# Optimization experiments

Measured on AMD Instinct MI355X. Metric: run time of the kernel, lower is better.

Reference implementation:

```python
import jax, jax.numpy as jnp
import numpy as np

B, N, D, E = 4, 16384, 128, 1048576  # batch, nodes/graph, hidden, total edges


def setup_inputs() -> dict:
    key = jax.random.key(0)
    k0, k1, k2, k3, k4, k5, k6 = jax.random.split(key, 7)
    x = jax.random.normal(k0, (B, N, D), dtype=jnp.float32)
    W = jax.random.normal(k1, (D, D), dtype=jnp.float32) * 0.05  # 'random_normal' init
    b = jax.random.normal(k2, (D,), dtype=jnp.float32) * 0.05
    edge_b = jax.random.randint(k3, (E,), 0, B, dtype=jnp.int32)
    edge_row = jax.random.randint(k4, (E,), 0, N, dtype=jnp.int32)
    edge_col = jax.random.randint(k5, (E,), 0, N, dtype=jnp.int32)
    edge_vals = jax.random.uniform(k6, (E,), dtype=jnp.float32)
    return {"x": x, "W": W, "b": b, "edge_b": edge_b, "edge_row": edge_row,
            "edge_col": edge_col, "edge_vals": edge_vals, "k": 2}


def reference(x, W, b, edge_b, edge_row, edge_col, edge_vals, k):
    # adj is a batched sparse [B, N, N]; edges stored as (batch, row, col, val) COO.
    seg_row = edge_b * N + edge_row  # flattened destination id in [0, B*N)
    # in_degrees = sum_j |adj[b, i, j]|
    deg = jax.ops.segment_sum(jnp.abs(edge_vals), seg_row, num_segments=B * N)
    deg = deg.reshape(B, N)
    norm = jnp.power(deg + 1e-6, -0.5)[..., None]          # [B, N, 1]
    norm_k = jnp.power(norm, k)                             # computed but unused (faithful to source)
    support = jnp.einsum('bnd,de->bne', x, W)               # x @ W
    y = (support * norm).reshape(B * N, D)                  # pre-normalized features
    # SpMM: out[b, i] = sum_{(b,i,j)} adj_val * y[b, j]
    msgs = y[edge_b * N + edge_col] * edge_vals[:, None]    # [E, D] gather + scale
    agg = jax.ops.segment_sum(msgs, seg_row, num_segments=B * N).reshape(B, N, D)
    return jax.nn.relu(agg * norm + b)
```

## Files before the change

### kernel.cpp

```cpp
#include <hip/hip_runtime.h>
#include <stdint.h>

#define B_ 4
#define N_ 16384
#define D_ 128
#define E_ 1048576
#define BN_ 65536
#define NBKT 256
#define NBLK 256
#define SCANB 64

typedef __attribute__((ext_vector_type(8))) short short8;
typedef __attribute__((ext_vector_type(4))) float floatx4;

static constexpr size_t OFF_Y      = 0;
static constexpr size_t OFF_PACK2  = 16777216;
static constexpr size_t OFF_HIST   = OFF_PACK2 + 8388608;
static constexpr size_t OFF_CURSOR = OFF_HIST + 262144;
static constexpr size_t OFF_NORM   = OFF_CURSOR + 262144;
static constexpr size_t OFF_BSUM   = OFF_NORM + 262144;
static constexpr size_t OFF_WH     = OFF_BSUM + 1024;
static constexpr size_t OFF_WL     = OFF_WH + 32768;

__device__ __forceinline__ uint32_t rne16(uint32_t u) {
    return (u + 0x7FFFu + ((u >> 16) & 1u)) >> 16;
}
__device__ __forceinline__ void bf16split(float f, uint16_t& h, uint16_t& l) {
    uint32_t hb = rne16(__float_as_uint(f));
    h = (uint16_t)hb;
    float r = f - __uint_as_float(hb << 16);
    l = (uint16_t)rne16(__float_as_uint(r));
}

__global__ __launch_bounds__(1024) void k_hist(const int* __restrict__ eb,
                                               const int* __restrict__ er,
                                               const float* __restrict__ Wg,
                                               uint32_t* __restrict__ histM,
                                               uint16_t* __restrict__ WhG,
                                               uint16_t* __restrict__ WlG) {
    __shared__ uint32_t h[NBKT];
    int t = threadIdx.x;
    if (t < NBKT) h[t] = 0;
    __syncthreads();
    if (blockIdx.x < 16) {
        int g = blockIdx.x * 1024 + t;
        float w = Wg[g];
        uint16_t hh, ll;
        bf16split(w, hh, ll);
        int k = g >> 7, n = g & 127;
        int o = ((k >> 3) * 128 + n) * 8 + (k & 7);
        WhG[o] = hh;
        WlG[o] = ll;
    }
    int vbase = blockIdx.x * 1024 + t;
    int4 b4 = ((const int4*)eb)[vbase];
    int4 r4 = ((const int4*)er)[vbase];
    atomicAdd(&h[(uint32_t)(b4.x * N_ + r4.x) >> 8], 1u);
    atomicAdd(&h[(uint32_t)(b4.y * N_ + r4.y) >> 8], 1u);
    atomicAdd(&h[(uint32_t)(b4.z * N_ + r4.z) >> 8], 1u);
    atomicAdd(&h[(uint32_t)(b4.w * N_ + r4.w) >> 8], 1u);
    __syncthreads();
    if (t < NBKT) histM[t * NBLK + blockIdx.x] = h[t];
}

__global__ __launch_bounds__(1024) void k_scan1(uint32_t* __restrict__ histM,
                                                uint32_t* __restrict__ bsum) {
    __shared__ uint32_t s[1024];
    int t = threadIdx.x;
    int g = blockIdx.x * 1024 + t;
    uint32_t v = histM[g];
    s[t] = v;
    __syncthreads();
    for (int off = 1; off < 1024; off <<= 1) {
        uint32_t a = (t >= off) ? s[t - off] : 0u;
        __syncthreads();
        s[t] += a;
        __syncthreads();
    }
    histM[g] = s[t] - v;
    if (t == 1023) bsum[blockIdx.x] = s[1023];
}

__global__ void k_scan2(uint32_t* bsum) {
    if (threadIdx.x == 0) {
        uint32_t acc = 0;
        for (int i = 0; i < SCANB; ++i) { uint32_t v = bsum[i]; bsum[i] = acc; acc += v; }
    }
}

__global__ __launch_bounds__(1024) void k_scan3(uint32_t* __restrict__ histM,
                                                const uint32_t* __restrict__ bsum) {
    int g = blockIdx.x * 1024 + threadIdx.x;
    histM[g] += bsum[blockIdx.x];
}

__global__ __launch_bounds__(1024) void k_scatter(const int* __restrict__ eb,
                                                  const int* __restrict__ er,
                                                  const int* __restrict__ ec,
                                                  const float* __restrict__ ev,
                                                  const uint32_t* __restrict__ histM,
                                                  uint2* __restrict__ pack1) {
    __shared__ uint32_t cur[NBKT];
    int t = threadIdx.x;
    if (t < NBKT) cur[t] = histM[t * NBLK + blockIdx.x];
    __syncthreads();
    int vbase = blockIdx.x * 1024 + t;
    int4   b4 = ((const int4*)eb)[vbase];
    int4   r4 = ((const int4*)er)[vbase];
    int4   c4 = ((const int4*)ec)[vbase];
    float4 v4 = ((const float4*)ev)[vbase];
    {
        uint32_t key = (uint32_t)(b4.x * N_ + r4.x);
        uint32_t pos = atomicAdd(&cur[key >> 8], 1u);
        pack1[pos] = make_uint2(((key & 255u) << 14) | (uint32_t)c4.x, __float_as_uint(v4.x));
    }
    {
        uint32_t key = (uint32_t)(b4.y * N_ + r4.y);
        uint32_t pos = atomicAdd(&cur[key >> 8], 1u);
        pack1[pos] = make_uint2(((key & 255u) << 14) | (uint32_t)c4.y, __float_as_uint(v4.y));
    }
    {
        uint32_t key = (uint32_t)(b4.z * N_ + r4.z);
        uint32_t pos = atomicAdd(&cur[key >> 8], 1u);
        pack1[pos] = make_uint2(((key & 255u) << 14) | (uint32_t)c4.z, __float_as_uint(v4.z));
    }
    {
        uint32_t key = (uint32_t)(b4.w * N_ + r4.w);
        uint32_t pos = atomicAdd(&cur[key >> 8], 1u);
        pack1[pos] = make_uint2(((key & 255u) << 14) | (uint32_t)c4.w, __float_as_uint(v4.w));
    }
}

__global__ __launch_bounds__(1024) void k_build(const uint32_t* __restrict__ histM,
                                                const uint2* __restrict__ pack1,
                                                uint2* __restrict__ pack2,
                                                uint32_t* __restrict__ cursor,
                                                float* __restrict__ norm) {
    __shared__ uint32_t cnt[NBKT];
    __shared__ float    dsum[NBKT];
    __shared__ uint32_t scn[NBKT];
    __shared__ uint32_t rcur[NBKT];
    int t = threadIdx.x;
    int bkt = blockIdx.x;
    uint32_t bstart = histM[bkt * NBLK];
    uint32_t bend = (bkt == NBKT - 1) ? E_ : histM[(bkt + 1) * NBLK];
    if (t < NBKT) { cnt[t] = 0; dsum[t] = 0.f; }
    __syncthreads();
    for (uint32_t i = bstart + t; i < bend; i += 1024) {
        uint2 p = pack1[i];
        uint32_t nl = p.x >> 14;
        atomicAdd(&cnt[nl], 1u);
        atomicAdd(&dsum[nl], fabsf(__uint_as_float(p.y)));
    }
    __syncthreads();
    if (t < NBKT) scn[t] = cnt[t];
    __syncthreads();
    for (int off = 1; off < NBKT; off <<= 1) {
        uint32_t a = 0;
        if (t < NBKT && t >= off) a = scn[t - off];
        __syncthreads();
        if (t < NBKT) scn[t] += a;
        __syncthreads();
    }
    if (t < NBKT) {
        uint32_t incl = scn[t];
        uint32_t excl = incl - cnt[t];
        rcur[t] = bstart + excl;
        cursor[bkt * NBKT + t] = bstart + incl;
        norm[bkt * NBKT + t] = rsqrtf(dsum[t] + 1e-6f);
    }
    __syncthreads();
    uint32_t colbase = (uint32_t)(bkt >> 6) * N_;
    for (uint32_t i = bstart + t; i < bend; i += 1024) {
        uint2 p = pack1[i];
        uint32_t nl = p.x >> 14;
        uint32_t pos = atomicAdd(&rcur[nl], 1u);
        pack2[pos] = make_uint2(colbase + (p.x & 0x3FFFu), p.y);
    }
}

__global__ __launch_bounds__(256) void k_matmul_mfma(const float* __restrict__ x,
                                                     const uint16_t* __restrict__ WhG,
                                                     const uint16_t* __restrict__ WlG,
                                                     const float* __restrict__ norm,
                                                     uint32_t* __restrict__ ybf) {
    __shared__ short WhS[16384];
    __shared__ short WlS[16384];
    __shared__ short XhS[4096];
    __shared__ short XlS[4096];
    __shared__ float normS[32];
    int tid = threadIdx.x;
    int row0 = blockIdx.x * 32;

    {
        const uint4* whg = (const uint4*)WhG;
        const uint4* wlg = (const uint4*)WlG;
        uint4* whs = (uint4*)WhS;
        uint4* wls = (uint4*)WlS;
#pragma unroll
        for (int i = 0; i < 8; ++i) {
            whs[i * 256 + tid] = whg[i * 256 + tid];
            wls[i * 256 + tid] = wlg[i * 256 + tid];
        }
    }
#pragma unroll
    for (int cc = 0; cc < 2; ++cc) {
        int c = cc * 256 + tid;
        int m = c & 31, kk = c >> 5;
        const float4* xp = (const float4*)(x + (size_t)(row0 + m) * D_ + kk * 8);
        float4 f0 = xp[0], f1 = xp[1];
        union { short8 v; uint16_t s[8]; } uh, ul;
        bf16split(f0.x, uh.s[0], ul.s[0]); bf16split(f0.y, uh.s[1], ul.s[1]);
        bf16split(f0.z, uh.s[2], ul.s[2]); bf16split(f0.w, uh.s[3], ul.s[3]);
        bf16split(f1.x, uh.s[4], ul.s[4]); bf16split(f1.y, uh.s[5], ul.s[5]);
        bf16split(f1.z, uh.s[6], ul.s[6]); bf16split(f1.w, uh.s[7], ul.s[7]);
        ((short8*)XhS)[c] = uh.v;
        ((short8*)XlS)[c] = ul.v;
    }
    if (tid < 32) normS[tid] = norm[row0 + tid];
    __syncthreads();

    int lane = tid & 63;
    int wv = tid >> 6;
    int quad = lane >> 4;
    int l15 = lane & 15;
    int wcol0 = wv * 32;
    floatx4 acc[2][2] = {};
    const short8* Xh8 = (const short8*)XhS;
    const short8* Xl8 = (const short8*)XlS;
    const short8* Wh8 = (const short8*)WhS;
    const short8* Wl8 = (const short8*)WlS;
#pragma unroll
    for (int ks = 0; ks < 4; ++ks) {
        int kkq = ks * 4 + quad;
        short8 ah0 = Xh8[kkq * 32 + l15];
        short8 ah1 = Xh8[kkq * 32 + 16 + l15];
        short8 al0 = Xl8[kkq * 32 + l15];
        short8 al1 = Xl8[kkq * 32 + 16 + l15];
        short8 bh0 = Wh8[kkq * 128 + wcol0 + l15];
        short8 bh1 = Wh8[kkq * 128 + wcol0 + 16 + l15];
        short8 bl0 = Wl8[kkq * 128 + wcol0 + l15];
        short8 bl1 = Wl8[kkq * 128 + wcol0 + 16 + l15];
        acc[0][0] = __builtin_amdgcn_mfma_f32_16x16x32_bf16(ah0, bh0, acc[0][0], 0, 0, 0);
        acc[0][1] = __builtin_amdgcn_mfma_f32_16x16x32_bf16(ah0, bh1, acc[0][1], 0, 0, 0);
        acc[1][0] = __builtin_amdgcn_mfma_f32_16x16x32_bf16(ah1, bh0, acc[1][0], 0, 0, 0);
        acc[1][1] = __builtin_amdgcn_mfma_f32_16x16x32_bf16(ah1, bh1, acc[1][1], 0, 0, 0);
        acc[0][0] = __builtin_amdgcn_mfma_f32_16x16x32_bf16(ah0, bl0, acc[0][0], 0, 0, 0);
        acc[0][1] = __builtin_amdgcn_mfma_f32_16x16x32_bf16(ah0, bl1, acc[0][1], 0, 0, 0);
        acc[1][0] = __builtin_amdgcn_mfma_f32_16x16x32_bf16(ah1, bl0, acc[1][0], 0, 0, 0);
        acc[1][1] = __builtin_amdgcn_mfma_f32_16x16x32_bf16(ah1, bl1, acc[1][1], 0, 0, 0);
        acc[0][0] = __builtin_amdgcn_mfma_f32_16x16x32_bf16(al0, bh0, acc[0][0], 0, 0, 0);
        acc[0][1] = __builtin_amdgcn_mfma_f32_16x16x32_bf16(al0, bh1, acc[0][1], 0, 0, 0);
        acc[1][0] = __builtin_amdgcn_mfma_f32_16x16x32_bf16(al1, bh0, acc[1][0], 0, 0, 0);
        acc[1][1] = __builtin_amdgcn_mfma_f32_16x16x32_bf16(al1, bh1, acc[1][1], 0, 0, 0);
    }

#pragma unroll
    for (int rt = 0; rt < 2; ++rt) {
#pragma unroll
        for (int ct = 0; ct < 2; ++ct) {
            floatx4 v = acc[rt][ct];
            int rbase = rt * 16 + quad * 4;
            int cp = (wcol0 + ct * 16) / 2 + (l15 >> 1);
#pragma unroll
            for (int r = 0; r < 4; ++r) {
                float mine = v[r] * normS[rbase + r];
                float oth = __shfl_xor(mine, 1, 64);
                uint32_t a = __float_as_uint((lane & 1) ? oth : mine);
                uint32_t b = __float_as_uint((lane & 1) ? mine : oth);
                uint32_t packed = rne16(a) | (rne16(b) << 16);
                bool doit = ((lane & 1) == 0) ? (r < 2) : (r >= 2);
                if (doit)
                    ybf[(size_t)(row0 + rbase + r) * 64 + cp] = packed;
            }
        }
    }
}

__global__ __launch_bounds__(256) void k_spmm(const uint32_t* __restrict__ cursor,
                                              const uint2* __restrict__ pack,
                                              const uint32_t* __restrict__ ybf,
                                              const float* __restrict__ norm,
                                              const float* __restrict__ bias,
                                              float* __restrict__ out) {
    int node = blockIdx.x * 4 + (threadIdx.x >> 6);
    int lane = threadIdx.x & 63;
    uint32_t end = cursor[node];
    uint32_t start = (node == 0) ? 0u : cursor[node - 1];
    float2 a0 = {0.f,0.f}, a1 = {0.f,0.f}, a2 = {0.f,0.f}, a3 = {0.f,0.f};
    uint32_t e = start;
    for (; e + 8 <= end; e += 8) {
        uint2 p0 = pack[e + 0]; uint2 p1 = pack[e + 1];
        uint2 p2 = pack[e + 2]; uint2 p3 = pack[e + 3];
        uint2 p4 = pack[e + 4]; uint2 p5 = pack[e + 5];
        uint2 p6 = pack[e + 6]; uint2 p7 = pack[e + 7];
        uint32_t u0 = ybf[(size_t)p0.x * 64 + lane];
        uint32_t u1 = ybf[(size_t)p1.x * 64 + lane];
        uint32_t u2 = ybf[(size_t)p2.x * 64 + lane];
        uint32_t u3 = ybf[(size_t)p3.x * 64 + lane];
        uint32_t u4 = ybf[(size_t)p4.x * 64 + lane];
        uint32_t u5 = ybf[(size_t)p5.x * 64 + lane];
        uint32_t u6 = ybf[(size_t)p6.x * 64 + lane];
        uint32_t u7 = ybf[(size_t)p7.x * 64 + lane];
        float v0 = __uint_as_float(p0.y), v1 = __uint_as_float(p1.y);
        float v2 = __uint_as_float(p2.y), v3 = __uint_as_float(p3.y);
        float v4 = __uint_as_float(p4.y), v5 = __uint_as_float(p5.y);
        float v6 = __uint_as_float(p6.y), v7 = __uint_as_float(p7.y);
        a0.x = fmaf(v0, __uint_as_float(u0 << 16), a0.x);
        a0.y = fmaf(v0, __uint_as_float(u0 & 0xFFFF0000u), a0.y);
        a1.x = fmaf(v1, __uint_as_float(u1 << 16), a1.x);
        a1.y = fmaf(v1, __uint_as_float(u1 & 0xFFFF0000u), a1.y);
        a2.x = fmaf(v2, __uint_as_float(u2 << 16), a2.x);
        a2.y = fmaf(v2, __uint_as_float(u2 & 0xFFFF0000u), a2.y);
        a3.x = fmaf(v3, __uint_as_float(u3 << 16), a3.x);
        a3.y = fmaf(v3, __uint_as_float(u3 & 0xFFFF0000u), a3.y);
        a0.x = fmaf(v4, __uint_as_float(u4 << 16), a0.x);
        a0.y = fmaf(v4, __uint_as_float(u4 & 0xFFFF0000u), a0.y);
        a1.x = fmaf(v5, __uint_as_float(u5 << 16), a1.x);
        a1.y = fmaf(v5, __uint_as_float(u5 & 0xFFFF0000u), a1.y);
        a2.x = fmaf(v6, __uint_as_float(u6 << 16), a2.x);
        a2.y = fmaf(v6, __uint_as_float(u6 & 0xFFFF0000u), a2.y);
        a3.x = fmaf(v7, __uint_as_float(u7 << 16), a3.x);
        a3.y = fmaf(v7, __uint_as_float(u7 & 0xFFFF0000u), a3.y);
    }
    for (; e + 4 <= end; e += 4) {
        uint2 p0 = pack[e + 0]; uint2 p1 = pack[e + 1];
        uint2 p2 = pack[e + 2]; uint2 p3 = pack[e + 3];
        uint32_t u0 = ybf[(size_t)p0.x * 64 + lane];
        uint32_t u1 = ybf[(size_t)p1.x * 64 + lane];
        uint32_t u2 = ybf[(size_t)p2.x * 64 + lane];
        uint32_t u3 = ybf[(size_t)p3.x * 64 + lane];
        float v0 = __uint_as_float(p0.y), v1 = __uint_as_float(p1.y);
        float v2 = __uint_as_float(p2.y), v3 = __uint_as_float(p3.y);
        a0.x = fmaf(v0, __uint_as_float(u0 << 16), a0.x);
        a0.y = fmaf(v0, __uint_as_float(u0 & 0xFFFF0000u), a0.y);
        a1.x = fmaf(v1, __uint_as_float(u1 << 16), a1.x);
        a1.y = fmaf(v1, __uint_as_float(u1 & 0xFFFF0000u), a1.y);
        a2.x = fmaf(v2, __uint_as_float(u2 << 16), a2.x);
        a2.y = fmaf(v2, __uint_as_float(u2 & 0xFFFF0000u), a2.y);
        a3.x = fmaf(v3, __uint_as_float(u3 << 16), a3.x);
        a3.y = fmaf(v3, __uint_as_float(u3 & 0xFFFF0000u), a3.y);
    }
    for (; e < end; ++e) {
        uint2 p = pack[e];
        float v = __uint_as_float(p.y);
        uint32_t u = ybf[(size_t)p.x * 64 + lane];
        a0.x = fmaf(v, __uint_as_float(u << 16), a0.x);
        a0.y = fmaf(v, __uint_as_float(u & 0xFFFF0000u), a0.y);
    }
    float2 acc;
    acc.x = (a0.x + a1.x) + (a2.x + a3.x);
    acc.y = (a0.y + a1.y) + (a2.y + a3.y);
    float nm = norm[node];
    float2 bb = ((const float2*)bias)[lane];
    float2 o;
    o.x = fmaxf(fmaf(acc.x, nm, bb.x), 0.f);
    o.y = fmaxf(fmaf(acc.y, nm, bb.y), 0.f);
    ((float2*)out)[(size_t)node * 64 + lane] = o;
}

extern "C" void kernel_launch(void* const* d_in, const int* in_sizes, int n_in,
                              void* d_out, int out_size, void* d_ws, size_t ws_size,
                              hipStream_t stream) {
    const float* x  = (const float*)d_in[0];
    const float* W  = (const float*)d_in[1];
    const float* bi = (const float*)d_in[2];
    const int* eb   = (const int*)d_in[3];
    const int* er   = (const int*)d_in[4];
    const int* ec   = (const int*)d_in[5];
    const float* ev = (const float*)d_in[6];
    float* out = (float*)d_out;

    char* ws = (char*)d_ws;
    uint32_t* ybf    = (uint32_t*)(ws + OFF_Y);
    uint2*    pack1  = (uint2*)(ws + OFF_Y);
    uint2*    pack2  = (uint2*)(ws + OFF_PACK2);
    uint32_t* histM  = (uint32_t*)(ws + OFF_HIST);
    uint32_t* cursor = (uint32_t*)(ws + OFF_CURSOR);
    float*    norm   = (float*)(ws + OFF_NORM);
    uint32_t* bsum   = (uint32_t*)(ws + OFF_BSUM);
    uint16_t* WhG    = (uint16_t*)(ws + OFF_WH);
    uint16_t* WlG    = (uint16_t*)(ws + OFF_WL);

    k_hist   <<<NBLK,  1024, 0, stream>>>(eb, er, W, histM, WhG, WlG);
    k_scan1  <<<SCANB, 1024, 0, stream>>>(histM, bsum);
    k_scan2  <<<1,     64,   0, stream>>>(bsum);
    k_scan3  <<<SCANB, 1024, 0, stream>>>(histM, bsum);
    k_scatter<<<NBLK,  1024, 0, stream>>>(eb, er, ec, ev, histM, pack1);
    k_build  <<<NBKT,  1024, 0, stream>>>(histM, pack1, pack2, cursor, norm);
    k_matmul_mfma<<<BN_ / 32, 256, 0, stream>>>(x, WhG, WlG, norm, ybf);
    k_spmm   <<<BN_ / 4, 256, 0, stream>>>(cursor, pack2, ybf, norm, bi, out);
}
```

Baseline: 201.4 us.

## Fold scan3 into consumers and gather 16-byte rows with four edges per wavefront

```diff
diff --git a/kernel.cpp b/kernel.cpp
--- a/kernel.cpp
+++ b/kernel.cpp
@@ -88,21 +88,16 @@
     }
 }
 
-__global__ __launch_bounds__(1024) void k_scan3(uint32_t* __restrict__ histM,
-                                                const uint32_t* __restrict__ bsum) {
-    int g = blockIdx.x * 1024 + threadIdx.x;
-    histM[g] += bsum[blockIdx.x];
-}
-
 __global__ __launch_bounds__(1024) void k_scatter(const int* __restrict__ eb,
                                                   const int* __restrict__ er,
                                                   const int* __restrict__ ec,
                                                   const float* __restrict__ ev,
                                                   const uint32_t* __restrict__ histM,
+                                                  const uint32_t* __restrict__ bsum,
                                                   uint2* __restrict__ pack1) {
     __shared__ uint32_t cur[NBKT];
     int t = threadIdx.x;
-    if (t < NBKT) cur[t] = histM[t * NBLK + blockIdx.x];
+    if (t < NBKT) cur[t] = histM[t * NBLK + blockIdx.x] + bsum[t >> 2];
     __syncthreads();
     int vbase = blockIdx.x * 1024 + t;
     int4   b4 = ((const int4*)eb)[vbase];
@@ -132,6 +127,7 @@
 }
 
 __global__ __launch_bounds__(1024) void k_build(const uint32_t* __restrict__ histM,
+                                                const uint32_t* __restrict__ bsum,
                                                 const uint2* __restrict__ pack1,
                                                 uint2* __restrict__ pack2,
                                                 uint32_t* __restrict__ cursor,
@@ -142,8 +138,9 @@
     __shared__ uint32_t rcur[NBKT];
     int t = threadIdx.x;
     int bkt = blockIdx.x;
-    uint32_t bstart = histM[bkt * NBLK];
-    uint32_t bend = (bkt == NBKT - 1) ? E_ : histM[(bkt + 1) * NBLK];
+    uint32_t bstart = histM[bkt * NBLK] + bsum[bkt >> 2];
+    uint32_t bend = (bkt == NBKT - 1) ? E_
+                    : histM[(bkt + 1) * NBLK] + bsum[(bkt + 1) >> 2];
     if (t < NBKT) { cnt[t] = 0; dsum[t] = 0.f; }
     __syncthreads();
     for (uint32_t i = bstart + t; i < bend; i += 1024) {
@@ -277,86 +274,73 @@
     }
 }
 
+__device__ __forceinline__ void fma8(float* acc, float v, uint4 u) {
+    acc[0] = fmaf(v, __uint_as_float(u.x << 16), acc[0]);
+    acc[1] = fmaf(v, __uint_as_float(u.x & 0xFFFF0000u), acc[1]);
+    acc[2] = fmaf(v, __uint_as_float(u.y << 16), acc[2]);
+    acc[3] = fmaf(v, __uint_as_float(u.y & 0xFFFF0000u), acc[3]);
+    acc[4] = fmaf(v, __uint_as_float(u.z << 16), acc[4]);
+    acc[5] = fmaf(v, __uint_as_float(u.z & 0xFFFF0000u), acc[5]);
+    acc[6] = fmaf(v, __uint_as_float(u.w << 16), acc[6]);
+    acc[7] = fmaf(v, __uint_as_float(u.w & 0xFFFF0000u), acc[7]);
+}
+
 __global__ __launch_bounds__(256) void k_spmm(const uint32_t* __restrict__ cursor,
                                               const uint2* __restrict__ pack,
-                                              const uint32_t* __restrict__ ybf,
+                                              const uint4* __restrict__ y4,
                                               const float* __restrict__ norm,
                                               const float* __restrict__ bias,
                                               float* __restrict__ out) {
     int node = blockIdx.x * 4 + (threadIdx.x >> 6);
     int lane = threadIdx.x & 63;
+    int esub = lane >> 4;
+    int chunk = lane & 15;
     uint32_t end = cursor[node];
     uint32_t start = (node == 0) ? 0u : cursor[node - 1];
-    float2 a0 = {0.f,0.f}, a1 = {0.f,0.f}, a2 = {0.f,0.f}, a3 = {0.f,0.f};
+    float acc[8] = {0.f,0.f,0.f,0.f,0.f,0.f,0.f,0.f};
     uint32_t e = start;
-    for (; e + 8 <= end; e += 8) {
-        uint2 p0 = pack[e + 0]; uint2 p1 = pack[e + 1];
-        uint2 p2 = pack[e + 2]; uint2 p3 = pack[e + 3];
-        uint2 p4 = pack[e + 4]; uint2 p5 = pack[e + 5];
-        uint2 p6 = pack[e + 6]; uint2 p7 = pack[e + 7];
-        uint32_t u0 = ybf[(size_t)p0.x * 64 + lane];
-        uint32_t u1 = ybf[(size_t)p1.x * 64 + lane];
-        uint32_t u2 = ybf[(size_t)p2.x * 64 + lane];
-        uint32_t u3 = ybf[(size_t)p3.x * 64 + lane];
-        uint32_t u4 = ybf[(size_t)p4.x * 64 + lane];
-        uint32_t u5 = ybf[(size_t)p5.x * 64 + lane];
-        uint32_t u6 = ybf[(size_t)p6.x * 64 + lane];
-        uint32_t u7 = ybf[(size_t)p7.x * 64 + lane];
-        float v0 = __uint_as_float(p0.y), v1 = __uint_as_float(p1.y);
-        float v2 = __uint_as_float(p2.y), v3 = __uint_as_float(p3.y);
-        float v4 = __uint_as_float(p4.y), v5 = __uint_as_float(p5.y);
-        float v6 = __uint_as_float(p6.y), v7 = __uint_as_float(p7.y);
-        a0.x = fmaf(v0, __uint_as_float(u0 << 16), a0.x);
-        a0.y = fmaf(v0, __uint_as_float(u0 & 0xFFFF0000u), a0.y);
-        a1.x = fmaf(v1, __uint_as_float(u1 << 16), a1.x);
-        a1.y = fmaf(v1, __uint_as_float(u1 & 0xFFFF0000u), a1.y);
-        a2.x = fmaf(v2, __uint_as_float(u2 << 16), a2.x);
-        a2.y = fmaf(v2, __uint_as_float(u2 & 0xFFFF0000u), a2.y);
-        a3.x = fmaf(v3, __uint_as_float(u3 << 16), a3.x);
-        a3.y = fmaf(v3, __uint_as_float(u3 & 0xFFFF0000u), a3.y);
-        a0.x = fmaf(v4, __uint_as_float(u4 << 16), a0.x);
-        a0.y = fmaf(v4, __uint_as_float(u4 & 0xFFFF0000u), a0.y);
-        a1.x = fmaf(v5, __uint_as_float(u5 << 16), a1.x);
-        a1.y = fmaf(v5, __uint_as_float(u5 & 0xFFFF0000u), a1.y);
-        a2.x = fmaf(v6, __uint_as_float(u6 << 16), a2.x);
-        a2.y = fmaf(v6, __uint_as_float(u6 & 0xFFFF0000u), a2.y);
-        a3.x = fmaf(v7, __uint_as_float(u7 << 16), a3.x);
-        a3.y = fmaf(v7, __uint_as_float(u7 & 0xFFFF0000u), a3.y);
+    for (; e + 16 <= end; e += 16) {
+        uint2 pa = pack[e + 0 + esub];
+        uint2 pb = pack[e + 4 + esub];
+        uint2 pc = pack[e + 8 + esub];
+        uint2 pd = pack[e + 12 + esub];
+        uint4 ua = y4[(size_t)pa.x * 16 + chunk];
+        uint4 ub = y4[(size_t)pb.x * 16 + chunk];
+        uint4 uc = y4[(size_t)pc.x * 16 + chunk];
+        uint4 ud = y4[(size_t)pd.x * 16 + chunk];
+        fma8(acc, __uint_as_float(pa.y), ua);
+        fma8(acc, __uint_as_float(pb.y), ub);
+        fma8(acc, __uint_as_float(pc.y), uc);
+        fma8(acc, __uint_as_float(pd.y), ud);
     }
     for (; e + 4 <= end; e += 4) {
-        uint2 p0 = pack[e + 0]; uint2 p1 = pack[e + 1];
-        uint2 p2 = pack[e + 2]; uint2 p3 = pack[e + 3];
-        uint32_t u0 = ybf[(size_t)p0.x * 64 + lane];
-        uint32_t u1 = ybf[(size_t)p1.x * 64 + lane];
-        uint32_t u2 = ybf[(size_t)p2.x * 64 + lane];
-        uint32_t u3 = ybf[(size_t)p3.x * 64 + lane];
-        float v0 = __uint_as_float(p0.y), v1 = __uint_as_float(p1.y);
-        float v2 = __uint_as_float(p2.y), v3 = __uint_as_float(p3.y);
-        a0.x = fmaf(v0, __uint_as_float(u0 << 16), a0.x);
-        a0.y = fmaf(v0, __uint_as_float(u0 & 0xFFFF0000u), a0.y);
-        a1.x = fmaf(v1, __uint_as_float(u1 << 16), a1.x);
-        a1.y = fmaf(v1, __uint_as_float(u1 & 0xFFFF0000u), a1.y);
-        a2.x = fmaf(v2, __uint_as_float(u2 << 16), a2.x);
-        a2.y = fmaf(v2, __uint_as_float(u2 & 0xFFFF0000u), a2.y);
-        a3.x = fmaf(v3, __uint_as_float(u3 << 16), a3.x);
-        a3.y = fmaf(v3, __uint_as_float(u3 & 0xFFFF0000u), a3.y);
-    }
-    for (; e < end; ++e) {
-        uint2 p = pack[e];
-        float v = __uint_as_float(p.y);
-        uint32_t u = ybf[(size_t)p.x * 64 + lane];
-        a0.x = fmaf(v, __uint_as_float(u << 16), a0.x);
-        a0.y = fmaf(v, __uint_as_float(u & 0xFFFF0000u), a0.y);
-    }
-    float2 acc;
-    acc.x = (a0.x + a1.x) + (a2.x + a3.x);
-    acc.y = (a0.y + a1.y) + (a2.y + a3.y);
-    float nm = norm[node];
-    float2 bb = ((const float2*)bias)[lane];
-    float2 o;
-    o.x = fmaxf(fmaf(acc.x, nm, bb.x), 0.f);
-    o.y = fmaxf(fmaf(acc.y, nm, bb.y), 0.f);
-    ((float2*)out)[(size_t)node * 64 + lane] = o;
+        uint2 p = pack[e + esub];
+        uint4 u = y4[(size_t)p.x * 16 + chunk];
+        fma8(acc, __uint_as_float(p.y), u);
+    }
+    if (e < end) {
+        uint32_t idx = e + esub;
+        bool act = idx < end;
+        uint2 p = pack[act ? idx : (end - 1)];
+        uint4 u = y4[(size_t)p.x * 16 + chunk];
+        float v = act ? __uint_as_float(p.y) : 0.f;
+        fma8(acc, v, u);
+    }
+#pragma unroll
+    for (int i = 0; i < 8; ++i) {
+        acc[i] += __shfl_xor(acc[i], 16, 64);
+        acc[i] += __shfl_xor(acc[i], 32, 64);
+    }
+    if (esub < 2) {
+        float nm = norm[node];
+        float4 bb = ((const float4*)bias)[chunk * 2 + esub];
+        float4 o;
+        o.x = fmaxf(fmaf(acc[esub * 4 + 0], nm, bb.x), 0.f);
+        o.y = fmaxf(fmaf(acc[esub * 4 + 1], nm, bb.y), 0.f);
+        o.z = fmaxf(fmaf(acc[esub * 4 + 2], nm, bb.z), 0.f);
+        o.w = fmaxf(fmaf(acc[esub * 4 + 3], nm, bb.w), 0.f);
+        ((float4*)out)[(size_t)node * 32 + chunk * 2 + esub] = o;
+    }
 }
 
 extern "C" void kernel_launch(void* const* d_in, const int* in_sizes, int n_in,
@@ -385,9 +369,8 @@
     k_hist   <<<NBLK,  1024, 0, stream>>>(eb, er, W, histM, WhG, WlG);
     k_scan1  <<<SCANB, 1024, 0, stream>>>(histM, bsum);
     k_scan2  <<<1,     64,   0, stream>>>(bsum);
-    k_scan3  <<<SCANB, 1024, 0, stream>>>(histM, bsum);
-    k_scatter<<<NBLK,  1024, 0, stream>>>(eb, er, ec, ev, histM, pack1);
-    k_build  <<<NBKT,  1024, 0, stream>>>(histM, pack1, pack2, cursor, norm);
+    k_scatter<<<NBLK,  1024, 0, stream>>>(eb, er, ec, ev, histM, bsum, pack1);
+    k_build  <<<NBKT,  1024, 0, stream>>>(histM, bsum, pack1, pack2, cursor, norm);
     k_matmul_mfma<<<BN_ / 32, 256, 0, stream>>>(x, WhG, WlG, norm, ybf);
-    k_spmm   <<<BN_ / 4, 256, 0, stream>>>(cursor, pack2, ybf, norm, bi, out);
-}
+    k_spmm   <<<BN_ / 4, 256, 0, stream>>>(cursor, pack2, (const uint4*)ybf, norm, bi, out);
+}
```

Result: faster. 188.4 us (-6.5%).
